# Performance work log

Hardware: AMD Instinct MI355X
Metric: run time of the kernel (lower is better)

The kernel has to match this reference:

```python
import jax, jax.numpy as jnp
import numpy as np

ALPHA = 0.929
BETA = 15.99
TAU = 0.0
EPS = 1e-8


def setup_inputs() -> dict:
    key = jax.random.key(0)
    k1, k2 = jax.random.split(key)
    head_outputs = jax.random.normal(k1, (8, 2048, 16, 128), dtype=jnp.float32)
    G = jax.random.normal(k2, (16, 16), dtype=jnp.float32)
    return {"head_outputs": head_outputs, "G": G}


def reference(head_outputs, G):
    B, T, H, d_h = head_outputs.shape
    N = B * T
    outputs = head_outputs.reshape(N, H, d_h)
    mu = outputs.mean(axis=0, keepdims=True)
    # torch .std() is unbiased (ddof=1)
    sigma = outputs.std(axis=0, keepdims=True, ddof=1)
    O_tilde = (outputs - mu) / (sigma + EPS)  # (N, H, d_h)

    # All pairwise cross-correlations in one batched contraction: (H, H, d_h, d_h)
    C = jnp.einsum('nid,nje->ijde', O_tilde, O_tilde) / N
    diff = C - jnp.eye(d_h, dtype=C.dtype)  # subtract_identity=True
    pair_loss = jnp.sum(diff * diff, axis=(2, 3))  # (H, H)

    w = ALPHA + (1.0 - ALPHA) * jax.nn.softplus(-BETA * (G - TAU))  # (H, H)

    upper = jnp.triu(jnp.ones((H, H), dtype=C.dtype), k=1)  # i < j mask
    n_pairs = H * (H - 1) // 2
    loss = jnp.sum(upper * w * pair_loss) / n_pairs
    return loss
```

## Files before the change

### kernel.cpp

```cpp
#include <hip/hip_runtime.h>
#include <hip/hip_bf16.h>

#define N_TOK   16384
#define HDIM    2048
#define NH      16
#define DH      128
#define NPAIRS  120
#define KCHUNKS 8
#define NKT     (N_TOK / 64)
#define KT_PER_CHUNK (NKT / KCHUNKS)
#define PANEL_BYTES 8192

#define SUM_OFF    0u
#define SUMSQ_OFF  8192u
#define MU_OFF     16384u
#define RINV_OFF   24576u
#define PC_OFF     36864u
#define XT_OFF     7901184u

typedef float     f32x4 __attribute__((ext_vector_type(4)));
typedef long long i64t;

#if __has_builtin(__builtin_amdgcn_cvt_pk_fp8_f32)
__device__ __forceinline__ unsigned pk4_fp8(float a, float b, float c, float d) {
    int w = __builtin_amdgcn_cvt_pk_fp8_f32(a, b, 0, false);
    w = __builtin_amdgcn_cvt_pk_fp8_f32(c, d, w, true);
    return (unsigned)w;
}
#else
__device__ __forceinline__ unsigned char f2e4m3_sw(float f) {
    unsigned u = __float_as_uint(f);
    unsigned s = (u >> 24) & 0x80u;
    unsigned a = u & 0x7fffffffu;
    if (a >= 0x43e00000u) return (unsigned char)(s | 0x7eu);
    if (a < 0x3c800000u) {
        float av = __uint_as_float(a);
        int q = (int)rintf(av * 512.0f);
        return (unsigned char)(s | (unsigned)q);
    }
    unsigned lsb = (a >> 20) & 1u;
    a += 0x7ffffu + lsb;
    int e8 = (int)(a >> 23) - 120;
    unsigned m = (a >> 20) & 7u;
    return (unsigned char)(s | ((unsigned)e8 << 3) | m);
}
__device__ __forceinline__ unsigned pk4_fp8(float a, float b, float c, float d) {
    return (unsigned)f2e4m3_sw(a) | ((unsigned)f2e4m3_sw(b) << 8) |
           ((unsigned)f2e4m3_sw(c) << 16) | ((unsigned)f2e4m3_sw(d) << 24);
}
#endif

__global__ __launch_bounds__(256)
void stats_transpose_kernel(const float* __restrict__ X,
                            float* __restrict__ sum, float* __restrict__ sumsq,
                            unsigned char* __restrict__ Xt) {
    __shared__ float tile[64][129];
    __shared__ float sred[4][32][8];
    const int h  = blockIdx.x;
    const int by = blockIdx.y;
    const int n0 = by * 64;
    const int tx = threadIdx.x;
    const int w  = tx >> 6, l = tx & 63;
    const int cq = tx & 31;
    const int rq0 = tx >> 5;

    float4 s  = make_float4(0.f, 0.f, 0.f, 0.f);
    float4 ss = make_float4(0.f, 0.f, 0.f, 0.f);
    #pragma unroll
    for (int it = 0; it < 8; ++it) {
        int r = it * 8 + rq0;
        float4 x = *(const float4*)(X + (size_t)(n0 + r) * HDIM + h * DH + cq * 4);
        s.x += x.x; s.y += x.y; s.z += x.z; s.w += x.w;
        ss.x += x.x * x.x; ss.y += x.y * x.y; ss.z += x.z * x.z; ss.w += x.w * x.w;
        tile[r][cq * 4 + 0] = x.x; tile[r][cq * 4 + 1] = x.y;
        tile[r][cq * 4 + 2] = x.z; tile[r][cq * 4 + 3] = x.w;
    }
    s.x += __shfl_down(s.x, 32);  s.y += __shfl_down(s.y, 32);
    s.z += __shfl_down(s.z, 32);  s.w += __shfl_down(s.w, 32);
    ss.x += __shfl_down(ss.x, 32); ss.y += __shfl_down(ss.y, 32);
    ss.z += __shfl_down(ss.z, 32); ss.w += __shfl_down(ss.w, 32);
    if (l < 32) {
        sred[w][l][0] = s.x;  sred[w][l][1] = s.y;
        sred[w][l][2] = s.z;  sred[w][l][3] = s.w;
        sred[w][l][4] = ss.x; sred[w][l][5] = ss.y;
        sred[w][l][6] = ss.z; sred[w][l][7] = ss.w;
    }
    __syncthreads();
    if (tx < 32) {
        float a0 = 0.f, a1 = 0.f, a2 = 0.f, a3 = 0.f;
        float b0 = 0.f, b1 = 0.f, b2 = 0.f, b3 = 0.f;
        #pragma unroll
        for (int w2 = 0; w2 < 4; ++w2) {
            a0 += sred[w2][tx][0]; a1 += sred[w2][tx][1];
            a2 += sred[w2][tx][2]; a3 += sred[w2][tx][3];
            b0 += sred[w2][tx][4]; b1 += sred[w2][tx][5];
            b2 += sred[w2][tx][6]; b3 += sred[w2][tx][7];
        }
        int c = h * DH + tx * 4;
        atomicAdd(&sum[c + 0], a0);  atomicAdd(&sum[c + 1], a1);
        atomicAdd(&sum[c + 2], a2);  atomicAdd(&sum[c + 3], a3);
        atomicAdd(&sumsq[c + 0], b0); atomicAdd(&sumsq[c + 1], b1);
        atomicAdd(&sumsq[c + 2], b2); atomicAdd(&sumsq[c + 3], b3);
    }
    unsigned char* panel = Xt + ((size_t)h * NKT + by) * PANEL_BYTES;
    #pragma unroll
    for (int it = 0; it < 2; ++it) {
        int q = it * 256 + tx;
        int c = q >> 2, o = q & 3;
        uint4 pk;
        pk.x = pk4_fp8(tile[o*16+ 0][c], tile[o*16+ 1][c], tile[o*16+ 2][c], tile[o*16+ 3][c]);
        pk.y = pk4_fp8(tile[o*16+ 4][c], tile[o*16+ 5][c], tile[o*16+ 6][c], tile[o*16+ 7][c]);
        pk.z = pk4_fp8(tile[o*16+ 8][c], tile[o*16+ 9][c], tile[o*16+10][c], tile[o*16+11][c]);
        pk.w = pk4_fp8(tile[o*16+12][c], tile[o*16+13][c], tile[o*16+14][c], tile[o*16+15][c]);
        uint4 outv = ((c >> 3) & 1) ? make_uint4(pk.z, pk.w, pk.x, pk.y) : pk;
        *(uint4*)(panel + c * 64 + o * 16) = outv;
    }
}

__device__ __forceinline__ void gload16(const void* gsrc, void* ldst) {
    __builtin_amdgcn_global_load_lds(
        (const __attribute__((address_space(1))) unsigned int*)gsrc,
        (__attribute__((address_space(3))) unsigned int*)ldst,
        16, 0, 0);
}

__global__ __launch_bounds__(256, 4)
void gram_kernel(const unsigned char* __restrict__ Xt, float* __restrict__ pairC) {
    const int kc = blockIdx.x;
    const int p  = blockIdx.y;
    int i = 0, rem = p;
    while (rem >= NH - 1 - i) { rem -= NH - 1 - i; ++i; }
    const int j = i + 1 + rem;

    __shared__ alignas(16) unsigned char lds[2 * 2 * PANEL_BYTES];

    const int tx = threadIdx.x;
    const int w  = tx >> 6, l = tx & 63;
    const int wm = w >> 1, wn = w & 1;
    const int l15 = l & 15, quad = l >> 4;

    unsigned int goff0, goff1;
    {
        int r0 = tx >> 2, cl0 = tx & 3;
        goff0 = (unsigned int)(r0 * 64 + (cl0 ^ ((r0 >> 1) & 3)) * 16);
        int cfl = 256 + tx;
        int r1 = cfl >> 2, cl1 = cfl & 3;
        goff1 = (unsigned int)(r1 * 64 + (cl1 ^ ((r1 >> 1) & 3)) * 16);
    }
    const int lo0 = w * 1024;
    const int lo1 = 4096 + w * 1024;
    const char* Abase = (const char*)Xt + ((size_t)i * NKT + (size_t)kc * KT_PER_CHUNK) * PANEL_BYTES;
    const char* Bbase = (const char*)Xt + ((size_t)j * NKT + (size_t)kc * KT_PER_CHUNK) * PANEL_BYTES;

    f32x4 acc[4][4];
    #pragma unroll
    for (int mi = 0; mi < 4; ++mi)
        #pragma unroll
        for (int ni = 0; ni < 4; ++ni)
            acc[mi][ni] = (f32x4){0.f, 0.f, 0.f, 0.f};

    const int usw = (l15 & 6) | (l15 >> 3);

    {
        const char* pa = Abase;
        const char* pb = Bbase;
        char* base = (char*)lds;
        gload16(pa + goff0, base + lo0);
        gload16(pa + goff1, base + lo1);
        gload16(pb + goff0, base + 8192 + lo0);
        gload16(pb + goff1, base + 8192 + lo1);
    }
    asm volatile("s_waitcnt vmcnt(0)\n\ts_barrier" ::: "memory");

    int cur = 0;
    for (int kt = 0; kt < KT_PER_CHUNK; ++kt) {
        if (kt + 1 < KT_PER_CHUNK) {
            const char* pa = Abase + (size_t)(kt + 1) * PANEL_BYTES;
            const char* pb = Bbase + (size_t)(kt + 1) * PANEL_BYTES;
            char* base = (char*)lds + (cur ^ 1) * (2 * PANEL_BYTES);
            gload16(pa + goff0, base + lo0);
            gload16(pa + goff1, base + lo1);
            gload16(pb + goff0, base + 8192 + lo0);
            gload16(pb + goff1, base + 8192 + lo1);
        }

        const unsigned char* la = lds + cur * (2 * PANEL_BYTES);
        const unsigned char* lb = la + PANEL_BYTES;
        #pragma unroll
        for (int kh = 0; kh < 2; ++kh) {
            const int u = (kh * 4 + quad) ^ usw;
            i64t a[4], b[4];
            #pragma unroll
            for (int mi = 0; mi < 4; ++mi) {
                int r = wm * 64 + mi * 16 + l15;
                a[mi] = *(const i64t*)(la + r * 64 + u * 8);
            }
            #pragma unroll
            for (int ni = 0; ni < 4; ++ni) {
                int r = wn * 64 + ni * 16 + l15;
                b[ni] = *(const i64t*)(lb + r * 64 + u * 8);
            }
            #pragma unroll
            for (int mi = 0; mi < 4; ++mi)
                #pragma unroll
                for (int ni = 0; ni < 4; ++ni)
                    acc[mi][ni] = __builtin_amdgcn_mfma_f32_16x16x32_fp8_fp8(
                        a[mi], b[ni], acc[mi][ni], 0, 0, 0);
        }

        if (kt + 1 < KT_PER_CHUNK) {
            asm volatile("s_waitcnt vmcnt(0) lgkmcnt(0)\n\ts_barrier" ::: "memory");
        }
        cur ^= 1;
    }

    float* pc = pairC + (size_t)p * (DH * DH);
    #pragma unroll
    for (int mi = 0; mi < 4; ++mi)
        #pragma unroll
        for (int ni = 0; ni < 4; ++ni)
            #pragma unroll
            for (int r = 0; r < 4; ++r) {
                int row = wm * 64 + mi * 16 + quad * 4 + r;
                int col = wn * 64 + ni * 16 + l15;
                atomicAdd(&pc[row * DH + col], acc[mi][ni][r]);
            }
}

__global__ void pair_reduce_kernel(const float* __restrict__ pairC, const float* __restrict__ G,
                                   const float* __restrict__ sum, const float* __restrict__ sumsq,
                                   float* __restrict__ out) {
    int p = blockIdx.x;
    int i = 0, rem = p;
    while (rem >= NH - 1 - i) { rem -= NH - 1 - i; ++i; }
    int j = i + 1 + rem;
    __shared__ float smui[DH], smuj[DH], sri[DH], srj[DH];
    {
        int t = threadIdx.x;
        int head = (t < DH) ? i : j;
        int d = t & (DH - 1);
        int c = head * DH + d;
        float m = sum[c] * (1.f / (float)N_TOK);
        float var = (sumsq[c] - (float)N_TOK * m * m) * (1.f / (float)(N_TOK - 1));
        var = fmaxf(var, 0.f);
        float r = 1.f / (sqrtf(var) + 1e-8f);
        if (t < DH) { smui[d] = m; sri[d] = r; }
        else        { smuj[d] = m; srj[d] = r; }
    }
    __syncthreads();
    const float invN = 1.f / (float)N_TOK;
    const float* pc = pairC + (size_t)p * (DH * DH);
    float s = 0.f;
    for (int idx = threadIdx.x; idx < DH * DH; idx += 256) {
        int d = idx >> 7, e = idx & 127;
        float cn = (pc[idx] * invN - smui[d] * smuj[e]) * sri[d] * srj[e];
        float diff = cn - ((d == e) ? 1.f : 0.f);
        s += diff * diff;
    }
    for (int o = 32; o; o >>= 1) s += __shfl_down(s, o);
    __shared__ float red[4];
    if ((threadIdx.x & 63) == 0) red[threadIdx.x >> 6] = s;
    __syncthreads();
    if (threadIdx.x == 0) {
        float t = red[0] + red[1] + red[2] + red[3];
        float x = -15.99f * (G[i * NH + j] - 0.0f);
        float sp = (x > 20.f) ? x : log1pf(expf(x));
        float wgt = 0.929f + (1.f - 0.929f) * sp;
        atomicAdd(out, wgt * t * (1.f / (float)NPAIRS));
    }
}

extern "C" void kernel_launch(void* const* d_in, const int* in_sizes, int n_in,
                              void* d_out, int out_size, void* d_ws, size_t ws_size,
                              hipStream_t stream) {
    const float* X = (const float*)d_in[0];
    const float* G = (const float*)d_in[1];
    float* out = (float*)d_out;
    char* ws = (char*)d_ws;

    float*         sum   = (float*)(ws + SUM_OFF);
    float*         sumsq = (float*)(ws + SUMSQ_OFF);
    float*         pairC = (float*)(ws + PC_OFF);
    unsigned char* Xt    = (unsigned char*)(ws + XT_OFF);

    hipMemsetAsync(ws + SUM_OFF, 0, 16384, stream);
    hipMemsetAsync(ws + PC_OFF, 0, (size_t)NPAIRS * DH * DH * 4, stream);
    hipMemsetAsync(d_out, 0, 4, stream);

    stats_transpose_kernel<<<dim3(16, 256), 256, 0, stream>>>(X, sum, sumsq, Xt);
    gram_kernel<<<dim3(KCHUNKS, NPAIRS), 256, 0, stream>>>(Xt, pairC);
    pair_reduce_kernel<<<NPAIRS, 256, 0, stream>>>(pairC, G, sum, sumsq, out);
}
```

Baseline: 290.9 us.

## Use 16x16x128 scaled FP8 MFMA with 128-wide K tiles, dropping double buffering

Replaces the 16x16x32 FP8 MFMA with the MI355X 16x16x128 f8f6f4 scaled MFMA, using unit scale values of 0x7F. Each iteration now loads two 64-wide K panels for each of A and B, so the K step grows to 128. The double-buffered prefetch is removed: loads are issued and waited on before compute every iteration, so global latency is no longer overlapped with MFMA work. The intent is to cut MFMA instruction count and issue overhead at the cost of losing load/compute overlap.

```diff
diff --git a/kernel.cpp b/kernel.cpp
--- a/kernel.cpp
+++ b/kernel.cpp
@@ -9,16 +9,16 @@
 #define KCHUNKS 8
 #define NKT     (N_TOK / 64)
 #define KT_PER_CHUNK (NKT / KCHUNKS)
+#define KT128_PER_CHUNK (KT_PER_CHUNK / 2)
 #define PANEL_BYTES 8192
 
 #define SUM_OFF    0u
 #define SUMSQ_OFF  8192u
-#define MU_OFF     16384u
-#define RINV_OFF   24576u
 #define PC_OFF     36864u
 #define XT_OFF     7901184u
 
-typedef float     f32x4 __attribute__((ext_vector_type(4)));
+typedef float f32x4 __attribute__((ext_vector_type(4)));
+typedef int   v8i   __attribute__((ext_vector_type(8)));
 typedef long long i64t;
 
 #if __has_builtin(__builtin_amdgcn_cvt_pk_fp8_f32)
@@ -132,7 +132,7 @@
     while (rem >= NH - 1 - i) { rem -= NH - 1 - i; ++i; }
     const int j = i + 1 + rem;
 
-    __shared__ alignas(16) unsigned char lds[2 * 2 * PANEL_BYTES];
+    __shared__ alignas(16) unsigned char lds[4 * PANEL_BYTES];
 
     const int tx = threadIdx.x;
     const int w  = tx >> 6, l = tx & 63;
@@ -160,58 +160,62 @@
             acc[mi][ni] = (f32x4){0.f, 0.f, 0.f, 0.f};
 
     const int usw = (l15 & 6) | (l15 >> 3);
-
-    {
-        const char* pa = Abase;
-        const char* pb = Bbase;
-        char* base = (char*)lds;
-        gload16(pa + goff0, base + lo0);
-        gload16(pa + goff1, base + lo1);
-        gload16(pb + goff0, base + 8192 + lo0);
-        gload16(pb + goff1, base + 8192 + lo1);
-    }
-    asm volatile("s_waitcnt vmcnt(0)\n\ts_barrier" ::: "memory");
-
-    int cur = 0;
-    for (int kt = 0; kt < KT_PER_CHUNK; ++kt) {
-        if (kt + 1 < KT_PER_CHUNK) {
-            const char* pa = Abase + (size_t)(kt + 1) * PANEL_BYTES;
-            const char* pb = Bbase + (size_t)(kt + 1) * PANEL_BYTES;
-            char* base = (char*)lds + (cur ^ 1) * (2 * PANEL_BYTES);
-            gload16(pa + goff0, base + lo0);
-            gload16(pa + goff1, base + lo1);
-            gload16(pb + goff0, base + 8192 + lo0);
-            gload16(pb + goff1, base + 8192 + lo1);
-        }
-
-        const unsigned char* la = lds + cur * (2 * PANEL_BYTES);
-        const unsigned char* lb = la + PANEL_BYTES;
-        #pragma unroll
-        for (int kh = 0; kh < 2; ++kh) {
-            const int u = (kh * 4 + quad) ^ usw;
-            i64t a[4], b[4];
-            #pragma unroll
-            for (int mi = 0; mi < 4; ++mi) {
-                int r = wm * 64 + mi * 16 + l15;
-                a[mi] = *(const i64t*)(la + r * 64 + u * 8);
-            }
-            #pragma unroll
-            for (int ni = 0; ni < 4; ++ni) {
-                int r = wn * 64 + ni * 16 + l15;
-                b[ni] = *(const i64t*)(lb + r * 64 + u * 8);
-            }
+    const int selP = quad >> 1;
+    const int ub   = (quad & 1) * 4;
+    const int puo0 = ((ub + 0) ^ usw) * 8;
+    const int puo1 = ((ub + 1) ^ usw) * 8;
+    const int puo2 = ((ub + 2) ^ usw) * 8;
+    const int puo3 = ((ub + 3) ^ usw) * 8;
+    const unsigned char* laP = lds + selP * PANEL_BYTES;
+    const unsigned char* lbP = lds + 2 * PANEL_BYTES + selP * PANEL_BYTES;
+    const int rowA = (wm * 64 + l15) * 64;
+    const int rowB = (wn * 64 + l15) * 64;
+
+    for (int kt = 0; kt < KT128_PER_CHUNK; ++kt) {
+        {
+            const char* pa = Abase + (size_t)(kt * 2) * PANEL_BYTES;
+            const char* pb = Bbase + (size_t)(kt * 2) * PANEL_BYTES;
+            gload16(pa + goff0,               (char*)lds + lo0);
+            gload16(pa + goff1,               (char*)lds + lo1);
+            gload16(pa + PANEL_BYTES + goff0, (char*)lds + PANEL_BYTES + lo0);
+            gload16(pa + PANEL_BYTES + goff1, (char*)lds + PANEL_BYTES + lo1);
+            gload16(pb + goff0,               (char*)lds + 2 * PANEL_BYTES + lo0);
+            gload16(pb + goff1,               (char*)lds + 2 * PANEL_BYTES + lo1);
+            gload16(pb + PANEL_BYTES + goff0, (char*)lds + 3 * PANEL_BYTES + lo0);
+            gload16(pb + PANEL_BYTES + goff1, (char*)lds + 3 * PANEL_BYTES + lo1);
+        }
+        asm volatile("s_waitcnt vmcnt(0)\n\ts_barrier" ::: "memory");
+
+        v8i a[4];
+        #pragma unroll
+        for (int mi = 0; mi < 4; ++mi) {
+            const unsigned char* rp = laP + rowA + mi * 1024;
+            union { v8i v; i64t d[4]; } u;
+            u.d[0] = *(const i64t*)(rp + puo0);
+            u.d[1] = *(const i64t*)(rp + puo1);
+            u.d[2] = *(const i64t*)(rp + puo2);
+            u.d[3] = *(const i64t*)(rp + puo3);
+            a[mi] = u.v;
+        }
+        #pragma unroll
+        for (int ni = 0; ni < 4; ++ni) {
+            const unsigned char* rp = lbP + rowB + ni * 1024;
+            union { v8i v; i64t d[4]; } u;
+            u.d[0] = *(const i64t*)(rp + puo0);
+            u.d[1] = *(const i64t*)(rp + puo1);
+            u.d[2] = *(const i64t*)(rp + puo2);
+            u.d[3] = *(const i64t*)(rp + puo3);
+            v8i b = u.v;
             #pragma unroll
             for (int mi = 0; mi < 4; ++mi)
-                #pragma unroll
-                for (int ni = 0; ni < 4; ++ni)
-                    acc[mi][ni] = __builtin_amdgcn_mfma_f32_16x16x32_fp8_fp8(
-                        a[mi], b[ni], acc[mi][ni], 0, 0, 0);
-        }
-
-        if (kt + 1 < KT_PER_CHUNK) {
-            asm volatile("s_waitcnt vmcnt(0) lgkmcnt(0)\n\ts_barrier" ::: "memory");
-        }
-        cur ^= 1;
+                acc[mi][ni] = __builtin_amdgcn_mfma_scale_f32_16x16x128_f8f6f4(
+                    a[mi], b, acc[mi][ni], 0, 0,
+                    0, 0x7F7F7F7F, 0, 0x7F7F7F7F);
+        }
+
+        if (kt + 1 < KT128_PER_CHUNK) {
+            asm volatile("s_waitcnt lgkmcnt(0)\n\ts_barrier" ::: "memory");
+        }
     }
 
     float* pc = pairC + (size_t)p * (DH * DH);
```

After: 322.5 us. +10.9%, slower.
